# Kernel tuning notes

Hardware: AMD Instinct MI355X
Metric: run time of the kernel (lower is better)

## Reference

```python
import jax, jax.numpy as jnp
import numpy as np

N_NODES = 100000
N_EDGES = 1000000
N_GRAPHS = 16
CUTOFF = 6.0
ETAS = [0.5, 1.0, 2.0, 4.0]
OFFSETS = [0.0, 1.0, 2.0, 3.0, 4.0, 5.0, 6.0, 7.0]
SPECIES = (0, 1, 2)


def setup_inputs() -> dict:
    key = jax.random.key(0)
    ks = jax.random.split(key, 6)
    pos = jax.random.normal(ks[0], (N_NODES, 3), dtype=jnp.float32)
    cell = jax.random.normal(ks[1], (N_GRAPHS, 3, 3), dtype=jnp.float32)
    edge_shift = jax.random.normal(ks[2], (N_EDGES, 3), dtype=jnp.float32)
    z = jax.random.randint(ks[3], (N_NODES,), 0, 3, dtype=jnp.int64)
    edge_index = jax.random.randint(ks[4], (2, N_EDGES), 0, N_NODES, dtype=jnp.int64)
    batch = jnp.sort(jax.random.randint(ks[5], (N_NODES,), 0, N_GRAPHS, dtype=jnp.int64))
    # buffers from torch.cartesian_prod(etas, offsets).t(): etas repeated, offsets tiled
    etas = jnp.repeat(jnp.asarray(ETAS, dtype=jnp.float32), len(OFFSETS))      # [P]
    offsets = jnp.tile(jnp.asarray(OFFSETS, dtype=jnp.float32), len(ETAS))     # [P]
    return {"pos": pos, "cell": cell, "edge_shift": edge_shift, "etas": etas,
            "offsets": offsets, "z": z, "edge_index": edge_index, "batch": batch}


def reference(pos, cell, edge_shift, etas, offsets, z, edge_index, batch):
    i = edge_index[0]  # receiver
    j = edge_index[1]  # sender
    # periodic-image-shifted edge vectors: [E,3]
    vec_ij = pos[j] - pos[i] + jnp.einsum('ni,nij->nj', edge_shift, cell[batch[i]])
    r_ij = jnp.linalg.norm(vec_ij, axis=-1)  # [E]
    # cosine cutoff
    fc = jnp.where(r_ij < CUTOFF, 0.5 * (jnp.cos(jnp.pi * r_ij / CUTOFF) + 1.0), 0.0)
    # Gaussian RBF per (eta, offset) pair: [P, E]
    G2_ij = jnp.exp(-etas[:, None] * (r_ij - offsets[:, None]) ** 2 / CUTOFF ** 2) * fc
    zj = z[j]
    outs = []
    for sp in SPECIES:  # small fixed loop over species (3)
        m = (zj == sp).astype(G2_ij.dtype)          # [E]
        seg = jax.ops.segment_sum((G2_ij * m).T, i, num_segments=pos.shape[0])  # [N, P]
        outs.append(seg.T)                           # [P, N]
    return jnp.concatenate(outs, axis=0)             # [S*P, N]
```

## Files before the change

kernel.cpp:

```cpp
#include <hip/hip_runtime.h>
#include <math.h>

#define N_NODES 100000
#define N_EDGES 1000000
#define NPAIR 32
#define CUTOFF 6.0f

#define CHUNK 512
#define NCHUNK 196
#define CAP 8192
#define K1_THREADS 1024
#define EPT 4
#define EPB (K1_THREADS * EPT)
#define K1_BLOCKS ((N_EDGES + EPB - 1) / EPB)
#define AT 512
#define CURSTRIDE 16
#define NCUR (NCHUNK * CURSTRIDE)

__global__ __launch_bounds__(256) void pack_kernel(
    const float* __restrict__ pos,
    const int*   __restrict__ z,
    const int*   __restrict__ batch,
    float4*      __restrict__ packed,
    int*         __restrict__ cur)
{
    int n = blockIdx.x * 256 + threadIdx.x;
    if (n < NCUR) cur[n] = 0;
    if (n < N_NODES) {
        float4 p;
        p.x = pos[3 * n + 0];
        p.y = pos[3 * n + 1];
        p.z = pos[3 * n + 2];
        p.w = __int_as_float((z[n] & 3) | (batch[n] << 2));
        packed[n] = p;
    }
}

__global__ __launch_bounds__(1024) void bin_kernel(
    const float4* __restrict__ packed,
    const float*  __restrict__ cell,
    const float*  __restrict__ shift,
    const int*    __restrict__ ei,
    unsigned int* __restrict__ bucket,
    int*          __restrict__ cur)
{
    __shared__ int lhist[NCHUNK];
    __shared__ int lbase[NCHUNK];
    int tid = threadIdx.x;

    if (tid < NCHUNK) lhist[tid] = 0;
    __syncthreads();

    int base = blockIdx.x * EPB;

    int iv[EPT], jv[EPT];
    float sx[EPT], sy[EPT], sz[EPT];
    bool val[EPT];
#pragma unroll
    for (int q = 0; q < EPT; ++q) {
        int e = base + tid + q * K1_THREADS;
        val[q] = (e < N_EDGES);
        int ee = val[q] ? e : 0;
        iv[q] = ei[ee];
        jv[q] = ei[N_EDGES + ee];
        sx[q] = shift[3 * ee + 0];
        sy[q] = shift[3 * ee + 1];
        sz[q] = shift[3 * ee + 2];
    }

    float4 fi[EPT], fj[EPT];
#pragma unroll
    for (int q = 0; q < EPT; ++q) {
        fi[q] = packed[iv[q]];
        fj[q] = packed[jv[q]];
    }

    unsigned int recs[EPT];
    int chks[EPT], locs[EPT];
#pragma unroll
    for (int q = 0; q < EPT; ++q) {
        chks[q] = -1;
        if (val[q]) {
            int bi = __float_as_int(fi[q].w) >> 2;
            int zj = __float_as_int(fj[q].w) & 3;
            const float* C = cell + 9 * bi;
            float vx = fj[q].x - fi[q].x + sx[q] * C[0] + sy[q] * C[3] + sz[q] * C[6];
            float vy = fj[q].y - fi[q].y + sx[q] * C[1] + sy[q] * C[4] + sz[q] * C[7];
            float vz = fj[q].z - fi[q].z + sx[q] * C[2] + sy[q] * C[5] + sz[q] * C[8];
            float r = sqrtf(vx * vx + vy * vy + vz * vz);
            if (r < CUTOFF) {
                unsigned int qq = (unsigned int)(r * (2097152.0f / 6.0f));
                qq = min(qq, 2097151u);
                int c = iv[q] >> 9;
                recs[q] = (qq << 11) | ((unsigned int)(iv[q] & 511) << 2)
                        | (unsigned int)zj;
                chks[q] = c;
                locs[q] = atomicAdd(&lhist[c], 1);
            }
        }
    }
    __syncthreads();

    if (tid < NCHUNK) {
        int h  = lhist[tid];
        int hp = (h + 15) & ~15;
        lbase[tid] = (hp > 0) ? atomicAdd(&cur[tid * CURSTRIDE], hp) : 0;
    }
    __syncthreads();

#pragma unroll
    for (int q = 0; q < EPT; ++q) {
        if (chks[q] >= 0) {
            int slot = lbase[chks[q]] + locs[q];
            if (slot < CAP)
                bucket[(size_t)chks[q] * CAP + slot] = recs[q];
        }
    }

    if (tid < NCHUNK) {
        int h  = lhist[tid];
        int hp = (h + 15) & ~15;
        int b  = lbase[tid];
        for (int k = h; k < hp; ++k) {
            int slot = b + k;
            if (slot < CAP)
                bucket[(size_t)tid * CAP + slot] = 0xFFFFFFFFu;
        }
    }
}

__global__ __launch_bounds__(AT) void accum_kernel(
    const unsigned int* __restrict__ bucket,
    const int*          __restrict__ cur,
    float*              __restrict__ out)
{
    __shared__ unsigned int sorted[CAP];
    __shared__ int hist[CHUNK];
    __shared__ int lcur[CHUNK];
    int tid = threadIdx.x;
    int chunk = blockIdx.x;

    hist[tid] = 0;
    __syncthreads();

    int cnt = min(cur[chunk * CURSTRIDE], CAP);
    const unsigned int* b = bucket + (size_t)chunk * CAP;

    unsigned int regs[CAP / AT];
#pragma unroll
    for (int it = 0; it < CAP / AT; ++it) {
        int k = tid + it * AT;
        unsigned int rc = 0xFFFFFFFFu;
        if (k < cnt) rc = b[k];
        if ((rc & 3u) == 3u) rc = 0xFFFFFFFFu;
        else atomicAdd(&hist[(rc >> 2) & 511], 1);
        regs[it] = rc;
    }
    __syncthreads();

    int c0 = hist[tid];
    for (int d = 1; d < CHUNK; d <<= 1) {
        int y = (tid >= d) ? hist[tid - d] : 0;
        __syncthreads();
        hist[tid] += y;
        __syncthreads();
    }
    int incl = hist[tid];
    int beg  = incl - c0;
    lcur[tid] = beg;
    __syncthreads();

#pragma unroll
    for (int it = 0; it < CAP / AT; ++it) {
        unsigned int rc = regs[it];
        if (rc != 0xFFFFFFFFu) {
            int slot = atomicAdd(&lcur[(rc >> 2) & 511], 1);
            sorted[slot] = rc;
        }
    }
    __syncthreads();

    float a0[NPAIR], a1[NPAIR], a2[NPAIR];
#pragma unroll
    for (int p = 0; p < NPAIR; ++p) { a0[p] = 0.0f; a1[p] = 0.0f; a2[p] = 0.0f; }

    for (int k = beg; k < incl; ++k) {
        unsigned int rc = sorted[k];
        int spec = rc & 3;
        float r = (float)(rc >> 11) * (6.0f / 2097152.0f);
        float fc = 0.5f * (__cosf(r * (float)(M_PI / 6.0)) + 1.0f);
        float m0 = (spec == 0) ? fc : 0.0f;
        float m1 = (spec == 1) ? fc : 0.0f;
        float m2 = (spec == 2) ? fc : 0.0f;
#pragma unroll
        for (int o = 0; o < 8; ++o) {
            float d = r - (float)o;
            float e0 = __expf(d * d * (-0.5f / 36.0f));
            float e1 = e0 * e0;
            float e2 = e1 * e1;
            float e3 = e2 * e2;
            a0[o]      = fmaf(m0, e0, a0[o]);
            a1[o]      = fmaf(m1, e0, a1[o]);
            a2[o]      = fmaf(m2, e0, a2[o]);
            a0[8 + o]  = fmaf(m0, e1, a0[8 + o]);
            a1[8 + o]  = fmaf(m1, e1, a1[8 + o]);
            a2[8 + o]  = fmaf(m2, e1, a2[8 + o]);
            a0[16 + o] = fmaf(m0, e2, a0[16 + o]);
            a1[16 + o] = fmaf(m1, e2, a1[16 + o]);
            a2[16 + o] = fmaf(m2, e2, a2[16 + o]);
            a0[24 + o] = fmaf(m0, e3, a0[24 + o]);
            a1[24 + o] = fmaf(m1, e3, a1[24 + o]);
            a2[24 + o] = fmaf(m2, e3, a2[24 + o]);
        }
    }

    int node = chunk * CHUNK + tid;
    if (node < N_NODES) {
#pragma unroll
        for (int p = 0; p < NPAIR; ++p) {
            out[(size_t)(0 * NPAIR + p) * N_NODES + node] = a0[p];
            out[(size_t)(1 * NPAIR + p) * N_NODES + node] = a1[p];
            out[(size_t)(2 * NPAIR + p) * N_NODES + node] = a2[p];
        }
    }
}

extern "C" void kernel_launch(void* const* d_in, const int* in_sizes, int n_in,
                              void* d_out, int out_size, void* d_ws, size_t ws_size,
                              hipStream_t stream) {
    const float* pos   = (const float*)d_in[0];
    const float* cell  = (const float*)d_in[1];
    const float* shift = (const float*)d_in[2];
    const int*   z     = (const int*)d_in[5];
    const int*   ei    = (const int*)d_in[6];
    const int*   batch = (const int*)d_in[7];
    float* out = (float*)d_out;

    char* ws = (char*)d_ws;
    unsigned int* bucket = (unsigned int*)(ws);
    int*          cur    = (int*)(ws + 6422528);
    float4*       packed = (float4*)(ws + 6435072);

    int pblocks = (N_NODES + 255) / 256;
    pack_kernel<<<pblocks, 256, 0, stream>>>(pos, z, batch, packed, cur);

    bin_kernel<<<K1_BLOCKS, K1_THREADS, 0, stream>>>(packed, cell, shift, ei,
                                                     bucket, cur);
    accum_kernel<<<NCHUNK, AT, 0, stream>>>(bucket, cur, out);
}
```

Baseline: 57.17 us.

## Split accumulation per chunk into two half-chunk blocks with vectorized bucket reads

The accumulation kernel now launches two 256-thread blocks per 512-node chunk, each handling half the nodes. Both blocks read the whole chunk bucket twice with uint4 loads and keep only records for their own half, instead of holding records in registers. This raises block count from 196 to 392 so more CUs are busy and register pressure drops. The cost is redundant bucket reads, and a half that exceeds SCAP records silently drops the overflow.

```diff
diff --git a/kernel.cpp b/kernel.cpp
--- a/kernel.cpp
+++ b/kernel.cpp
@@ -13,9 +13,12 @@
 #define EPT 4
 #define EPB (K1_THREADS * EPT)
 #define K1_BLOCKS ((N_EDGES + EPB - 1) / EPB)
-#define AT 512
 #define CURSTRIDE 16
 #define NCUR (NCHUNK * CURSTRIDE)
+
+#define HCHUNK 256
+#define NHALF (NCHUNK * 2)
+#define SCAP 4608
 
 __global__ __launch_bounds__(256) void pack_kernel(
     const float* __restrict__ pos,
@@ -129,37 +132,42 @@
     }
 }
 
-__global__ __launch_bounds__(AT) void accum_kernel(
+__global__ __launch_bounds__(256) void accum_kernel(
     const unsigned int* __restrict__ bucket,
     const int*          __restrict__ cur,
     float*              __restrict__ out)
 {
-    __shared__ unsigned int sorted[CAP];
-    __shared__ int hist[CHUNK];
-    __shared__ int lcur[CHUNK];
+    __shared__ unsigned int sorted[SCAP];
+    __shared__ int hist[HCHUNK];
+    __shared__ int lcur[HCHUNK];
     int tid = threadIdx.x;
-    int chunk = blockIdx.x;
+    int chunk = blockIdx.x >> 1;
+    int half  = blockIdx.x & 1;
+    int locbase = half * HCHUNK;
 
     hist[tid] = 0;
     __syncthreads();
 
     int cnt = min(cur[chunk * CURSTRIDE], CAP);
-    const unsigned int* b = bucket + (size_t)chunk * CAP;
-
-    unsigned int regs[CAP / AT];
-#pragma unroll
-    for (int it = 0; it < CAP / AT; ++it) {
-        int k = tid + it * AT;
-        unsigned int rc = 0xFFFFFFFFu;
-        if (k < cnt) rc = b[k];
-        if ((rc & 3u) == 3u) rc = 0xFFFFFFFFu;
-        else atomicAdd(&hist[(rc >> 2) & 511], 1);
-        regs[it] = rc;
+    const uint4* b4 = (const uint4*)(bucket + (size_t)chunk * CAP);
+    int n4 = cnt >> 2;
+
+    for (int k = tid; k < n4; k += 256) {
+        uint4 v = b4[k];
+        unsigned int rr[4] = {v.x, v.y, v.z, v.w};
+#pragma unroll
+        for (int u = 0; u < 4; ++u) {
+            unsigned int rc = rr[u];
+            if ((rc & 3u) != 3u) {
+                int l = (int)((rc >> 2) & 511) - locbase;
+                if ((unsigned)l < HCHUNK) atomicAdd(&hist[l], 1);
+            }
+        }
     }
     __syncthreads();
 
     int c0 = hist[tid];
-    for (int d = 1; d < CHUNK; d <<= 1) {
+    for (int d = 1; d < HCHUNK; d <<= 1) {
         int y = (tid >= d) ? hist[tid - d] : 0;
         __syncthreads();
         hist[tid] += y;
@@ -170,12 +178,19 @@
     lcur[tid] = beg;
     __syncthreads();
 
-#pragma unroll
-    for (int it = 0; it < CAP / AT; ++it) {
-        unsigned int rc = regs[it];
-        if (rc != 0xFFFFFFFFu) {
-            int slot = atomicAdd(&lcur[(rc >> 2) & 511], 1);
-            sorted[slot] = rc;
+    for (int k = tid; k < n4; k += 256) {
+        uint4 v = b4[k];
+        unsigned int rr[4] = {v.x, v.y, v.z, v.w};
+#pragma unroll
+        for (int u = 0; u < 4; ++u) {
+            unsigned int rc = rr[u];
+            if ((rc & 3u) != 3u) {
+                int l = (int)((rc >> 2) & 511) - locbase;
+                if ((unsigned)l < HCHUNK) {
+                    int slot = atomicAdd(&lcur[l], 1);
+                    if (slot < SCAP) sorted[slot] = rc;
+                }
+            }
         }
     }
     __syncthreads();
@@ -214,7 +229,7 @@
         }
     }
 
-    int node = chunk * CHUNK + tid;
+    int node = chunk * CHUNK + locbase + tid;
     if (node < N_NODES) {
 #pragma unroll
         for (int p = 0; p < NPAIR; ++p) {
@@ -246,5 +261,5 @@
 
     bin_kernel<<<K1_BLOCKS, K1_THREADS, 0, stream>>>(packed, cell, shift, ei,
                                                      bucket, cur);
-    accum_kernel<<<NCHUNK, AT, 0, stream>>>(bucket, cur, out);
-}
+    accum_kernel<<<NHALF, 256, 0, stream>>>(bucket, cur, out);
+}
```

Result: no change. 57.85 us (+1.2%).
